# Optimization experiments

Hardware: AMD Instinct MI355X
Metric: run time of the kernel (lower is better)

Reference implementation:

```python
import jax, jax.numpy as jnp
import numpy as np

V, E, T_MAX, H, L = 20000, 384, 512, 8, 8
D = E // H  # head size 48
FF = 4 * E


def setup_inputs() -> dict:
    key = jax.random.key(0)
    ks = jax.random.split(key, 24)
    B, T = 16, 512
    s = 0.02
    return {
        "index": jax.random.randint(ks[0], (B, T), 0, V, dtype=jnp.int64),
        "targets": jax.random.randint(ks[1], (B, T), 0, V, dtype=jnp.int64),
        "tok_emb": s * jax.random.normal(ks[2], (V, E), jnp.float32),
        "pos_emb": s * jax.random.normal(ks[3], (T_MAX, E), jnp.float32),
        "Wq": s * jax.random.normal(ks[4], (L, E, H, D), jnp.float32),
        "bq": jnp.zeros((L, H, D), jnp.float32),
        "Wk": s * jax.random.normal(ks[5], (L, E, H, D), jnp.float32),
        "bk": jnp.zeros((L, H, D), jnp.float32),
        "Wv": s * jax.random.normal(ks[6], (L, E, H, D), jnp.float32),
        "bv": jnp.zeros((L, H, D), jnp.float32),
        "Wo": s * jax.random.normal(ks[7], (L, E, E), jnp.float32),
        "bo": jnp.zeros((L, E), jnp.float32),
        "ln1_g": jnp.ones((L, E), jnp.float32),
        "ln1_b": jnp.zeros((L, E), jnp.float32),
        "ln2_g": jnp.ones((L, E), jnp.float32),
        "ln2_b": jnp.zeros((L, E), jnp.float32),
        "W1": s * jax.random.normal(ks[8], (L, E, FF), jnp.float32),
        "b1": jnp.zeros((L, FF), jnp.float32),
        "W2": s * jax.random.normal(ks[9], (L, FF, E), jnp.float32),
        "b2": jnp.zeros((L, E), jnp.float32),
        "lnf_g": jnp.ones((E,), jnp.float32),
        "lnf_b": jnp.zeros((E,), jnp.float32),
        "lm_b": jnp.zeros((V,), jnp.float32),
    }


def layernorm(x, g, b, eps=1e-5):
    mu = jnp.mean(x, axis=-1, keepdims=True)
    var = jnp.var(x, axis=-1, keepdims=True)
    return (x - mu) * jax.lax.rsqrt(var + eps) * g + b


def reference(index, targets, tok_emb, pos_emb, Wq, bq, Wk, bk, Wv, bv, Wo, bo,
              ln1_g, ln1_b, ln2_g, ln2_b, W1, b1, W2, b2, lnf_g, lnf_b, lm_b):
    B, T = index.shape
    x = tok_emb[index] + pos_emb[:T]  # [B,T,E]
    causal = jnp.tril(jnp.ones((T, T), bool))
    scale = D ** -0.5
    for l in range(L):
        h = layernorm(x, ln1_g[l], ln1_b[l])
        q = jnp.einsum('bte,ehd->bthd', h, Wq[l]) + bq[l]
        k = jnp.einsum('bte,ehd->bthd', h, Wk[l]) + bk[l]
        v = jnp.einsum('bte,ehd->bthd', h, Wv[l]) + bv[l]
        scores = jnp.einsum('bqhd,bkhd->bhqk', q, k) * scale
        scores = jnp.where(causal, scores, -jnp.inf)
        w = jax.nn.softmax(scores, axis=-1)
        attn = jnp.einsum('bhqk,bkhd->bqhd', w, v).reshape(B, T, E)
        x = x + attn @ Wo[l] + bo[l]
        h2 = layernorm(x, ln2_g[l], ln2_b[l])
        ff = jax.nn.gelu(h2 @ W1[l] + b1[l], approximate=False) @ W2[l] + b2[l]
        x = x + ff
    x = layernorm(x, lnf_g, lnf_b)
    logits = x @ tok_emb.T + lm_b  # tied weights
    logits = logits.reshape(B * T, V)
    logp = jax.nn.log_softmax(logits, axis=-1)
    loss = -jnp.mean(jnp.take_along_axis(logp, targets.reshape(-1, 1), axis=-1))
    return logits, loss
```

## Files before the change

### kernel.cpp

```cpp
#include <hip/hip_runtime.h>
#include <hip/hip_bf16.h>
#include <math.h>

#define M_ROWS 8192
#define E_DIM 384
#define FF_DIM 1536
#define V_DIM 20000
#define VPAD 20096
#define N_LAYER 8
#define QK_SCALE 0.14433756729740643f
#define PSTRIDE 320

typedef __bf16 bf16x8 __attribute__((ext_vector_type(8)));
typedef short  s16x8  __attribute__((ext_vector_type(8)));
typedef float  f32x4  __attribute__((ext_vector_type(4)));
typedef __hip_bfloat16 bf16_t;

__device__ __forceinline__ void gl2lds16(const void* g, void* l) {
    __builtin_amdgcn_global_load_lds((const __attribute__((address_space(1))) void*)g,
                                     (__attribute__((address_space(3))) void*)l, 16, 0, 0);
}
__device__ __forceinline__ unsigned short bf16bits(float v) {
    return __builtin_bit_cast(unsigned short, __float2bfloat16(v));
}

__global__ __launch_bounds__(256) void tconv_kernel(
    const float* __restrict__ in, bf16_t* __restrict__ out,
    int K, int N, int outRows, int rowoff)
{
    __shared__ float tile[32][33];
    const int n0 = blockIdx.x * 32, k0 = blockIdx.y * 32;
    const float* ip = in + (size_t)blockIdx.z * K * N;
    bf16_t* op = out + (size_t)blockIdx.z * outRows * K;
    const int tx = threadIdx.x & 31, ty = threadIdx.x >> 5;
#pragma unroll
    for (int i = 0; i < 32; i += 8)
        tile[ty + i][tx] = ip[(size_t)(k0 + ty + i) * N + n0 + tx];
    __syncthreads();
#pragma unroll
    for (int i = 0; i < 32; i += 8)
        op[(size_t)(rowoff + n0 + ty + i) * K + k0 + tx] = __float2bfloat16(tile[tx][ty + i]);
}

__global__ __launch_bounds__(256) void tokconv_kernel(
    const float* __restrict__ tok, bf16_t* __restrict__ out)
{
    const size_t total = (size_t)VPAD * E_DIM;
    for (size_t i = blockIdx.x * 256ull + threadIdx.x; i < total; i += gridDim.x * 256ull) {
        int row = (int)(i / E_DIM);
        int col = (int)(i - (size_t)row * E_DIM);
        float v = (row < V_DIM) ? tok[(size_t)row * E_DIM + col] : 0.f;
        out[i] = __float2bfloat16(v);
    }
}

__global__ __launch_bounds__(256) void bqkv_kernel(
    const float* __restrict__ bq, const float* __restrict__ bk,
    const float* __restrict__ bv, float* __restrict__ o)
{
    int i = blockIdx.x * 256 + threadIdx.x;
    if (i < N_LAYER * 1152) {
        int l = i / 1152, c = i - l * 1152;
        float v = (c < 384) ? bq[l * 384 + c] : (c < 768) ? bk[l * 384 + c - 384] : bv[l * 384 + c - 768];
        o[i] = v;
    }
}

__global__ __launch_bounds__(256) void embed_kernel(
    const int* __restrict__ idx, const float* __restrict__ tok,
    const float* __restrict__ pos, float* __restrict__ x)
{
    int row = blockIdx.x * 4 + (threadIdx.x >> 6);
    int lane = threadIdx.x & 63;
    int t = row & 511;
    int id = idx[row];
    const float* tr = tok + (size_t)id * E_DIM;
    const float* pr = pos + (size_t)t * E_DIM;
    float* xr = x + (size_t)row * E_DIM;
#pragma unroll
    for (int i = 0; i < 6; i++) { int c = lane + i * 64; xr[c] = tr[c] + pr[c]; }
}

__global__ __launch_bounds__(256) void ln_kernel(
    const float* __restrict__ x, const float* __restrict__ g,
    const float* __restrict__ b, bf16_t* __restrict__ out)
{
    int row = blockIdx.x * 4 + (threadIdx.x >> 6);
    int lane = threadIdx.x & 63;
    const float* xr = x + (size_t)row * E_DIM;
    float vals[6];
    float s = 0.f;
#pragma unroll
    for (int i = 0; i < 6; i++) { vals[i] = xr[lane + i * 64]; s += vals[i]; }
#pragma unroll
    for (int off = 1; off < 64; off <<= 1) s += __shfl_xor(s, off);
    float mu = s * (1.f / E_DIM);
    float sq = 0.f;
#pragma unroll
    for (int i = 0; i < 6; i++) { float d = vals[i] - mu; sq += d * d; }
#pragma unroll
    for (int off = 1; off < 64; off <<= 1) sq += __shfl_xor(sq, off);
    float rstd = rsqrtf(sq * (1.f / E_DIM) + 1e-5f);
    bf16_t* orow = out + (size_t)row * E_DIM;
#pragma unroll
    for (int i = 0; i < 6; i++) {
        int c = lane + i * 64;
        orow[c] = __float2bfloat16((vals[i] - mu) * rstd * g[c] + b[c]);
    }
}

template <int MODE, int MREP, bool SWAP>
__global__ __launch_bounds__(256) void gemm_kernel(
    const bf16_t* __restrict__ A, const bf16_t* __restrict__ Bt,
    const float* __restrict__ bias, void* __restrict__ Cv, void* __restrict__ C2,
    int Ncols, int K)
{
    constexpr int BMR = MREP * 32;
    __shared__ __align__(16) short smem[8192];
    const int t = threadIdx.x;
    const int w = t >> 6, lane = t & 63;
    const int wm = w >> 1, wn = w & 1;
    const int bm = (MODE == 3 ? blockIdx.x : blockIdx.y) * BMR;
    const int bn = (MODE == 3 ? blockIdx.y : blockIdx.x) * 128;

    f32x4 acc[MREP][4];
#pragma unroll
    for (int m = 0; m < MREP; m++)
#pragma unroll
        for (int n = 0; n < 4; n++)
            acc[m][n] = (f32x4){0.f, 0.f, 0.f, 0.f};

    const int lg = lane >> 4;
    const int ll = lane & 15;

    for (int kt = 0; kt < K; kt += 32) {
        __syncthreads();
#pragma unroll
        for (int i = 0; i < MREP / 2; i++) {
            int li = i * 256 + t;
            int g = li >> (MREP == 4 ? 7 : 6);
            int row = li & (BMR - 1);
            gl2lds16(A + (size_t)(bm + row) * K + kt + g * 8,
                     smem + (size_t)(i * 256 + w * 64) * 8);
        }
#pragma unroll
        for (int i = 0; i < 2; i++) {
            int li = i * 256 + t;
            gl2lds16(Bt + (size_t)(bn + (li & 127)) * K + kt + (li >> 7) * 8,
                     smem + 4096 + (size_t)(i * 256 + w * 64) * 8);
        }
        asm volatile("s_waitcnt vmcnt(0)" ::: "memory");
        __syncthreads();

        bf16x8 af[MREP], bfr[4];
#pragma unroll
        for (int m = 0; m < MREP; m++)
            af[m] = __builtin_bit_cast(bf16x8,
                *(const s16x8*)&smem[(lg * BMR + wm * (BMR / 2) + m * 16 + ll) * 8]);
#pragma unroll
        for (int n = 0; n < 4; n++)
            bfr[n] = __builtin_bit_cast(bf16x8,
                *(const s16x8*)&smem[4096 + (lg * 128 + wn * 64 + n * 16 + ll) * 8]);
#pragma unroll
        for (int m = 0; m < MREP; m++)
#pragma unroll
            for (int n = 0; n < 4; n++) {
                if (SWAP)
                    acc[m][n] = __builtin_amdgcn_mfma_f32_16x16x32_bf16(bfr[n], af[m], acc[m][n], 0, 0, 0);
                else
                    acc[m][n] = __builtin_amdgcn_mfma_f32_16x16x32_bf16(af[m], bfr[n], acc[m][n], 0, 0, 0);
            }
    }

    if constexpr (SWAP) {
        const int rowm0 = bm + wm * (BMR / 2) + ll;
        const int coln0 = bn + wn * 64 + lg * 4;

        if constexpr (MODE == 4) {
            bf16_t* qkvb = (bf16_t*)Cv;
            const float sc = (bn >= 384) ? 1.f : QK_SCALE;
#pragma unroll
            for (int n = 0; n < 4; n++) {
                const int coln = coln0 + n * 16;
                const float4 b4 = *(const float4*)&bias[coln];
#pragma unroll
                for (int m = 0; m < MREP; m++) {
                    const int row = rowm0 + m * 16;
                    ushort4 pk;
                    pk.x = bf16bits((acc[m][n][0] + b4.x) * sc);
                    pk.y = bf16bits((acc[m][n][1] + b4.y) * sc);
                    pk.z = bf16bits((acc[m][n][2] + b4.z) * sc);
                    pk.w = bf16bits((acc[m][n][3] + b4.w) * sc);
                    *(ushort4*)&qkvb[(size_t)row * 1152 + coln] = pk;
                }
            }
        } else if constexpr (MODE == 1) {
            float* C = (float*)Cv;
#pragma unroll
            for (int n = 0; n < 4; n++) {
                const int coln = coln0 + n * 16;
                const float4 b4 = *(const float4*)&bias[coln];
#pragma unroll
                for (int m = 0; m < MREP; m++) {
                    const int row = rowm0 + m * 16;
                    float4 cv = *(float4*)&C[(size_t)row * Ncols + coln];
                    cv.x += acc[m][n][0] + b4.x;
                    cv.y += acc[m][n][1] + b4.y;
                    cv.z += acc[m][n][2] + b4.z;
                    cv.w += acc[m][n][3] + b4.w;
                    *(float4*)&C[(size_t)row * Ncols + coln] = cv;
                }
            }
        } else if constexpr (MODE == 2) {
            bf16_t* O = (bf16_t*)Cv;
#pragma unroll
            for (int n = 0; n < 4; n++) {
                const int coln = coln0 + n * 16;
                const float4 b4 = *(const float4*)&bias[coln];
#pragma unroll
                for (int m = 0; m < MREP; m++) {
                    const int row = rowm0 + m * 16;
                    float v0 = acc[m][n][0] + b4.x, v1 = acc[m][n][1] + b4.y;
                    float v2 = acc[m][n][2] + b4.z, v3 = acc[m][n][3] + b4.w;
                    v0 = 0.5f * v0 * (1.f + erff(v0 * 0.70710678118654752f));
                    v1 = 0.5f * v1 * (1.f + erff(v1 * 0.70710678118654752f));
                    v2 = 0.5f * v2 * (1.f + erff(v2 * 0.70710678118654752f));
                    v3 = 0.5f * v3 * (1.f + erff(v3 * 0.70710678118654752f));
                    ushort4 pk;
                    pk.x = bf16bits(v0); pk.y = bf16bits(v1);
                    pk.z = bf16bits(v2); pk.w = bf16bits(v3);
                    *(ushort4*)&O[(size_t)row * Ncols + coln] = pk;
                }
            }
        } else if constexpr (MODE == 3) {
            float* C = (float*)Cv;
            float* pbuf = (float*)C2;
            const int ptile = blockIdx.y * 2 + wn;
#pragma unroll
            for (int m = 0; m < MREP; m++) {
                const int row = rowm0 + m * 16;
                float se = 0.f;
#pragma unroll
                for (int n = 0; n < 4; n++) {
                    const int coln = coln0 + n * 16;
                    if (coln + 3 < Ncols) {
                        const float4 b4 = *(const float4*)&bias[coln];
                        float4 v;
                        v.x = acc[m][n][0] + b4.x;
                        v.y = acc[m][n][1] + b4.y;
                        v.z = acc[m][n][2] + b4.z;
                        v.w = acc[m][n][3] + b4.w;
                        *(float4*)&C[(size_t)row * Ncols + coln] = v;
                        se += __expf(v.x) + __expf(v.y) + __expf(v.z) + __expf(v.w);
                    } else {
#pragma unroll
                        for (int e = 0; e < 4; e++) {
                            int col = coln + e;
                            if (col < Ncols) {
                                float v = acc[m][n][e] + bias[col];
                                C[(size_t)row * Ncols + col] = v;
                                se += __expf(v);
                            }
                        }
                    }
                }
                se += __shfl_xor(se, 16);
                se += __shfl_xor(se, 32);
                if (lg == 0) pbuf[(size_t)row * PSTRIDE + ptile] = se;
            }
        }
        return;
    }

    {
        const int r0 = bm + wm * (BMR / 2) + lg * 4;
        const int c0 = bn + wn * 64 + ll;
        bf16_t* vtb = (bf16_t*)C2;
#pragma unroll
        for (int n = 0; n < 4; n++) {
            const int col = c0 + n * 16;
            const float bv = bias[col];
            const int hh = col / 48, dd = col - hh * 48;
#pragma unroll
            for (int m = 0; m < MREP; m++) {
                const int row0 = r0 + m * 16;
                const int bb = row0 >> 9, tt2 = row0 & 511;
                ushort4 pk;
                pk.x = bf16bits(acc[m][n][0] + bv);
                pk.y = bf16bits(acc[m][n][1] + bv);
                pk.z = bf16bits(acc[m][n][2] + bv);
                pk.w = bf16bits(acc[m][n][3] + bv);
                *(ushort4*)&vtb[((size_t)(bb * 8 + hh) * 48 + dd) * 512 + tt2] = pk;
            }
        }
    }
}

__global__ __launch_bounds__(256) void attn_kernel(
    const bf16_t* __restrict__ qkvb, const bf16_t* __restrict__ vt,
    bf16_t* __restrict__ o)
{
    const int qt = blockIdx.x, bh = blockIdx.y;
    const int b = bh >> 3, h = bh & 7;
    __shared__ unsigned short psm[4608];
    const int tid = threadIdx.x;
    const int w = tid >> 6, lane = tid & 63;
    const int ll = lane & 15, g = lane >> 4;
    const int q0 = qt * 64;
    const int q_abs = q0 + ll * 4 + w;

    const bf16_t* qrow = qkvb + (size_t)(b * 512 + q_abs) * 1152 + h * 48;
    bf16x8 qf0 = __builtin_bit_cast(bf16x8, *(const s16x8*)(qrow + g * 8));
    bf16x8 qf1 = {};
    if (g < 2) qf1 = __builtin_bit_cast(bf16x8, *(const s16x8*)(qrow + 32 + g * 8));

    f32x4 oacc[3];
#pragma unroll
    for (int df = 0; df < 3; df++) oacc[df] = (f32x4){0.f, 0.f, 0.f, 0.f};
    float mrun = -1e30f, ssum = 0.f;

    const bf16_t* kb0 = qkvb + (size_t)b * 512 * 1152 + 384 + h * 48;
    const bf16_t* vb0 = vt + (size_t)bh * 48 * 512;
    const int ntiles = 2 * (qt + 1);

    for (int kt = 0; kt < ntiles; kt++) {
        const int kbase = kt * 32;
        f32x4 sfr[2];
#pragma unroll
        for (int f = 0; f < 2; f++) {
            const bf16_t* krow = kb0 + (size_t)(kbase + f * 16 + ll) * 1152;
            bf16x8 k0 = __builtin_bit_cast(bf16x8, *(const s16x8*)(krow + g * 8));
            bf16x8 k1 = {};
            if (g < 2) k1 = __builtin_bit_cast(bf16x8, *(const s16x8*)(krow + 32 + g * 8));
            f32x4 z = {0.f, 0.f, 0.f, 0.f};
            z = __builtin_amdgcn_mfma_f32_16x16x32_bf16(k0, qf0, z, 0, 0, 0);
            z = __builtin_amdgcn_mfma_f32_16x16x32_bf16(k1, qf1, z, 0, 0, 0);
            sfr[f] = z;
        }
        bf16x8 vf[3];
#pragma unroll
        for (int df = 0; df < 3; df++)
            vf[df] = __builtin_bit_cast(bf16x8,
                *(const s16x8*)(vb0 + (size_t)(df * 16 + ll) * 512 + kbase + g * 8));

        float p[8];
        float tmax = -1e30f;
#pragma unroll
        for (int f = 0; f < 2; f++)
#pragma unroll
            for (int j = 0; j < 4; j++) {
                int key = kbase + f * 16 + g * 4 + j;
                float sv = sfr[f][j];
                sv = (key > q_abs) ? -1e30f : sv;
                p[f * 4 + j] = sv;
                tmax = fmaxf(tmax, sv);
            }
        tmax = fmaxf(tmax, __shfl_xor(tmax, 16));
        tmax = fmaxf(tmax, __shfl_xor(tmax, 32));
        float mnew = fmaxf(mrun, tmax);
        float corr = __expf(mrun - mnew);
        float psum = 0.f;
#pragma unroll
        for (int i = 0; i < 8; i++) { p[i] = __expf(p[i] - mnew); psum += p[i]; }
        psum += __shfl_xor(psum, 16);
        psum += __shfl_xor(psum, 32);
        ssum = ssum * corr + psum;
        mrun = mnew;
#pragma unroll
        for (int df = 0; df < 3; df++)
#pragma unroll
            for (int j = 0; j < 4; j++) oacc[df][j] *= corr;

        const int pbase = (w * 2 + (kt & 1)) * 576;
#pragma unroll
        for (int f = 0; f < 2; f++)
#pragma unroll
            for (int j = 0; j < 4; j++)
                psm[pbase + (f * 16 + g * 4 + j) * 18 + ll] =
                    __builtin_bit_cast(unsigned short, __float2bfloat16(p[f * 4 + j]));
        s16x8 pr;
#pragma unroll
        for (int i = 0; i < 8; i++)
            pr[i] = (short)psm[pbase + (g * 8 + i) * 18 + ll];
        bf16x8 pf = __builtin_bit_cast(bf16x8, pr);
#pragma unroll
        for (int df = 0; df < 3; df++)
            oacc[df] = __builtin_amdgcn_mfma_f32_16x16x32_bf16(vf[df], pf, oacc[df], 0, 0, 0);
    }

    float inv = 1.f / ssum;
    bf16_t* orow = o + (size_t)(b * 512 + q_abs) * 384 + h * 48;
#pragma unroll
    for (int df = 0; df < 3; df++) {
        ushort4 pk;
        pk.x = bf16bits(oacc[df][0] * inv);
        pk.y = bf16bits(oacc[df][1] * inv);
        pk.z = bf16bits(oacc[df][2] * inv);
        pk.w = bf16bits(oacc[df][3] * inv);
        *(ushort4*)&orow[df * 16 + g * 4] = pk;
    }
}

__global__ __launch_bounds__(256) void loss_row2_kernel(
    const float* __restrict__ pbuf, const float* __restrict__ logits,
    const int* __restrict__ targets, float* __restrict__ rowloss)
{
    int row = blockIdx.x * 4 + (threadIdx.x >> 6);
    int lane = threadIdx.x & 63;
    const float* pr = pbuf + (size_t)row * PSTRIDE;
    float s = 0.f;
    for (int i = lane; i < 314; i += 64) s += pr[i];
#pragma unroll
    for (int off = 1; off < 64; off <<= 1) s += __shfl_xor(s, off);
    if (lane == 0) {
        int tgt = targets[row];
        rowloss[row] = logf(s) - logits[(size_t)row * V_DIM + tgt];
    }
}

__global__ __launch_bounds__(256) void loss_reduce_kernel(
    const float* __restrict__ rowloss, float* __restrict__ out)
{
    int t = threadIdx.x;
    __shared__ float red[4];
    float s = 0.f;
    for (int i = t; i < M_ROWS; i += 256) s += rowloss[i];
#pragma unroll
    for (int off = 1; off < 64; off <<= 1) s += __shfl_xor(s, off);
    if ((t & 63) == 0) red[t >> 6] = s;
    __syncthreads();
    if (t == 0) out[0] = (red[0] + red[1] + red[2] + red[3]) * (1.f / M_ROWS);
}

extern "C" void kernel_launch(void* const* d_in, const int* in_sizes, int n_in,
                              void* d_out, int out_size, void* d_ws, size_t ws_size,
                              hipStream_t stream)
{
    const int*   index   = (const int*)d_in[0];
    const int*   targets = (const int*)d_in[1];
    const float* tok_emb = (const float*)d_in[2];
    const float* pos_emb = (const float*)d_in[3];
    const float* Wq = (const float*)d_in[4];
    const float* bq = (const float*)d_in[5];
    const float* Wk = (const float*)d_in[6];
    const float* bk = (const float*)d_in[7];
    const float* Wv = (const float*)d_in[8];
    const float* bv = (const float*)d_in[9];
    const float* Wo = (const float*)d_in[10];
    const float* bo = (const float*)d_in[11];
    const float* ln1_g = (const float*)d_in[12];
    const float* ln1_b = (const float*)d_in[13];
    const float* ln2_g = (const float*)d_in[14];
    const float* ln2_b = (const float*)d_in[15];
    const float* W1 = (const float*)d_in[16];
    const float* b1 = (const float*)d_in[17];
    const float* W2 = (const float*)d_in[18];
    const float* b2 = (const float*)d_in[19];
    const float* lnf_g = (const float*)d_in[20];
    const float* lnf_b = (const float*)d_in[21];
    const float* lm_b  = (const float*)d_in[22];

    float* out = (float*)d_out;
    char* wsb = (char*)d_ws;

    float*  x     = (float*)(wsb + 0);
    bf16_t* hbuf  = (bf16_t*)(wsb + 12582912);
    bf16_t* obuf  = (bf16_t*)(wsb + 18874368);
    bf16_t* qkvb  = (bf16_t*)(wsb + 25165824);
    bf16_t* vtb   = (bf16_t*)(wsb + 44040192);
    bf16_t* ffmid = (bf16_t*)(wsb + 18874368);
    bf16_t* tokb  = (bf16_t*)(wsb + 50331648);
    bf16_t* qkvw  = (bf16_t*)(wsb + 65765376);
    bf16_t* wo_t  = (bf16_t*)(wsb + 72843264);
    bf16_t* w1_t  = (bf16_t*)(wsb + 75202560);
    bf16_t* w2_t  = (bf16_t*)(wsb + 84639744);
    float*  bqkv  = (float*)(wsb + 94076928);
    float*  rowloss = (float*)(wsb + 94113792);
    float*  pbuf  = (float*)(wsb + 94146560);

    tokconv_kernel<<<2048, 256, 0, stream>>>(tok_emb, tokb);
    tconv_kernel<<<dim3(12, 12, 8), 256, 0, stream>>>(Wq, qkvw, 384, 384, 1152, 0);
    tconv_kernel<<<dim3(12, 12, 8), 256, 0, stream>>>(Wk, qkvw, 384, 384, 1152, 384);
    tconv_kernel<<<dim3(12, 12, 8), 256, 0, stream>>>(Wv, qkvw, 384, 384, 1152, 768);
    tconv_kernel<<<dim3(12, 12, 8), 256, 0, stream>>>(Wo, wo_t, 384, 384, 384, 0);
    tconv_kernel<<<dim3(48, 12, 8), 256, 0, stream>>>(W1, w1_t, 384, 1536, 1536, 0);
    tconv_kernel<<<dim3(12, 48, 8), 256, 0, stream>>>(W2, w2_t, 1536, 384, 384, 0);
    bqkv_kernel<<<36, 256, 0, stream>>>(bq, bk, bv, bqkv);

    embed_kernel<<<2048, 256, 0, stream>>>(index, tok_emb, pos_emb, x);

    for (int l = 0; l < N_LAYER; l++) {
        const bf16_t* qkvw_l = qkvw + (size_t)l * 1152 * 384;
        const float*  bqkv_l = bqkv + l * 1152;
        ln_kernel<<<2048, 256, 0, stream>>>(x, ln1_g + l * E_DIM, ln1_b + l * E_DIM, hbuf);
        gemm_kernel<4, 4, true><<<dim3(6, 64), 256, 0, stream>>>(
            hbuf, qkvw_l, bqkv_l, qkvb, nullptr, 1152, 384);
        gemm_kernel<5, 4, false><<<dim3(3, 64), 256, 0, stream>>>(
            hbuf, qkvw_l + (size_t)768 * 384, bqkv_l + 768, nullptr, vtb, 384, 384);
        attn_kernel<<<dim3(8, 128), 256, 0, stream>>>(qkvb, vtb, obuf);
        gemm_kernel<1, 2, true><<<dim3(3, 128), 256, 0, stream>>>(
            obuf, wo_t + (size_t)l * 384 * 384, bo + l * E_DIM, x, nullptr, 384, 384);
        ln_kernel<<<2048, 256, 0, stream>>>(x, ln2_g + l * E_DIM, ln2_b + l * E_DIM, hbuf);
        gemm_kernel<2, 4, true><<<dim3(12, 64), 256, 0, stream>>>(
            hbuf, w1_t + (size_t)l * 1536 * 384, b1 + l * FF_DIM, ffmid, nullptr, 1536, 384);
        gemm_kernel<1, 2, true><<<dim3(3, 128), 256, 0, stream>>>(
            ffmid, w2_t + (size_t)l * 384 * 1536, b2 + l * E_DIM, x, nullptr, 384, 1536);
    }

    ln_kernel<<<2048, 256, 0, stream>>>(x, lnf_g, lnf_b, hbuf);
    gemm_kernel<3, 4, true><<<dim3(64, 157), 256, 0, stream>>>(
        hbuf, tokb, lm_b, out, pbuf, V_DIM, 384);

    loss_row2_kernel<<<2048, 256, 0, stream>>>(pbuf, out, targets, rowloss);
    loss_reduce_kernel<<<1, 256, 0, stream>>>(rowloss, out + (size_t)M_ROWS * V_DIM);
}
```

Measured before the change: 1.995 ms.

## Add dedicated logits kernel keeping A tile resident in LDS across vocab tiles

Replaces the generic GEMM for the final vocab projection with a kernel that loads the full 64x384 row block of normalized activations into LDS once, then loops over up to four 128-column vocab tiles, streaming only the tied-embedding tiles. The fused bias, logit store and per-tile exp-sum partials are kept, now written per wave, which doubles the partial count, so the row-loss kernel sums more entries. The partial-sum buffer moves into a reused workspace region. The aim is to cut repeated A reloads and raise reuse. The cost is 64KB of LDS per block, which limits occupancy, and no overlap of loads with compute.

```diff
diff --git a/kernel.cpp b/kernel.cpp
--- a/kernel.cpp
+++ b/kernel.cpp
@@ -9,7 +9,8 @@
 #define VPAD 20096
 #define N_LAYER 8
 #define QK_SCALE 0.14433756729740643f
-#define PSTRIDE 320
+#define PSTRIDE 640
+#define NPART 628
 
 typedef __bf16 bf16x8 __attribute__((ext_vector_type(8)));
 typedef short  s16x8  __attribute__((ext_vector_type(8)));
@@ -120,8 +121,8 @@
     const int t = threadIdx.x;
     const int w = t >> 6, lane = t & 63;
     const int wm = w >> 1, wn = w & 1;
-    const int bm = (MODE == 3 ? blockIdx.x : blockIdx.y) * BMR;
-    const int bn = (MODE == 3 ? blockIdx.y : blockIdx.x) * 128;
+    const int bm = blockIdx.y * BMR;
+    const int bn = blockIdx.x * 128;
 
     f32x4 acc[MREP][4];
 #pragma unroll
@@ -232,42 +233,6 @@
                     *(ushort4*)&O[(size_t)row * Ncols + coln] = pk;
                 }
             }
-        } else if constexpr (MODE == 3) {
-            float* C = (float*)Cv;
-            float* pbuf = (float*)C2;
-            const int ptile = blockIdx.y * 2 + wn;
-#pragma unroll
-            for (int m = 0; m < MREP; m++) {
-                const int row = rowm0 + m * 16;
-                float se = 0.f;
-#pragma unroll
-                for (int n = 0; n < 4; n++) {
-                    const int coln = coln0 + n * 16;
-                    if (coln + 3 < Ncols) {
-                        const float4 b4 = *(const float4*)&bias[coln];
-                        float4 v;
-                        v.x = acc[m][n][0] + b4.x;
-                        v.y = acc[m][n][1] + b4.y;
-                        v.z = acc[m][n][2] + b4.z;
-                        v.w = acc[m][n][3] + b4.w;
-                        *(float4*)&C[(size_t)row * Ncols + coln] = v;
-                        se += __expf(v.x) + __expf(v.y) + __expf(v.z) + __expf(v.w);
-                    } else {
-#pragma unroll
-                        for (int e = 0; e < 4; e++) {
-                            int col = coln + e;
-                            if (col < Ncols) {
-                                float v = acc[m][n][e] + bias[col];
-                                C[(size_t)row * Ncols + col] = v;
-                                se += __expf(v);
-                            }
-                        }
-                    }
-                }
-                se += __shfl_xor(se, 16);
-                se += __shfl_xor(se, 32);
-                if (lg == 0) pbuf[(size_t)row * PSTRIDE + ptile] = se;
-            }
         }
         return;
     }
@@ -296,6 +261,108 @@
     }
 }
 
+__global__ __launch_bounds__(256) void logits_kernel(
+    const bf16_t* __restrict__ A, const bf16_t* __restrict__ Bt,
+    const float* __restrict__ bias, float* __restrict__ C,
+    float* __restrict__ pbuf)
+{
+    __shared__ __align__(16) short smem[32768];
+    const int t = threadIdx.x;
+    const int w = t >> 6, lane = t & 63;
+    const int lg = lane >> 4, ll = lane & 15;
+    const int bm = blockIdx.x * 64;
+    const int bnsup = blockIdx.y;
+    const int bn0 = bnsup * 512;
+    const int ntiles = (bnsup < 39) ? 4 : 1;
+
+#pragma unroll
+    for (int i = 0; i < 12; i++) {
+        int c = i * 256 + t;
+        int kg = c >> 6, row = c & 63;
+        gl2lds16(A + (size_t)(bm + row) * E_DIM + kg * 8,
+                 smem + (size_t)(i * 256 + w * 64) * 8);
+    }
+    asm volatile("s_waitcnt vmcnt(0)" ::: "memory");
+    __syncthreads();
+
+    short* smB = smem + 24576;
+    for (int bnl = 0; bnl < ntiles; bnl++) {
+        const int tb = bn0 + bnl * 128;
+        f32x4 acc[4][2];
+#pragma unroll
+        for (int m = 0; m < 4; m++)
+#pragma unroll
+            for (int nf = 0; nf < 2; nf++)
+                acc[m][nf] = (f32x4){0.f, 0.f, 0.f, 0.f};
+
+        for (int kt = 0; kt < 6; kt++) {
+            __syncthreads();
+#pragma unroll
+            for (int i = 0; i < 4; i++) {
+                int c = i * 256 + t;
+                int kg = c >> 7, col = c & 127;
+                gl2lds16(Bt + (size_t)(tb + col) * E_DIM + kt * 64 + kg * 8,
+                         smB + (size_t)(i * 256 + w * 64) * 8);
+            }
+            asm volatile("s_waitcnt vmcnt(0)" ::: "memory");
+            __syncthreads();
+#pragma unroll
+            for (int kk = 0; kk < 2; kk++) {
+                bf16x8 af[4], bfr[2];
+#pragma unroll
+                for (int m = 0; m < 4; m++)
+                    af[m] = __builtin_bit_cast(bf16x8,
+                        *(const s16x8*)&smem[((kt * 8 + kk * 4 + lg) * 64 + m * 16 + ll) * 8]);
+#pragma unroll
+                for (int nf = 0; nf < 2; nf++)
+                    bfr[nf] = __builtin_bit_cast(bf16x8,
+                        *(const s16x8*)&smB[((kk * 4 + lg) * 128 + w * 32 + nf * 16 + ll) * 8]);
+#pragma unroll
+                for (int m = 0; m < 4; m++)
+#pragma unroll
+                    for (int nf = 0; nf < 2; nf++)
+                        acc[m][nf] = __builtin_amdgcn_mfma_f32_16x16x32_bf16(
+                            bfr[nf], af[m], acc[m][nf], 0, 0, 0);
+            }
+        }
+
+        const int cn0 = tb + w * 32 + lg * 4;
+        const int pidx = bnsup * 16 + bnl * 4 + w;
+#pragma unroll
+        for (int m = 0; m < 4; m++) {
+            const int row = bm + m * 16 + ll;
+            float se = 0.f;
+#pragma unroll
+            for (int nf = 0; nf < 2; nf++) {
+                const int cn = cn0 + nf * 16;
+                if (cn + 3 < V_DIM) {
+                    const float4 b4 = *(const float4*)&bias[cn];
+                    float4 v;
+                    v.x = acc[m][nf][0] + b4.x;
+                    v.y = acc[m][nf][1] + b4.y;
+                    v.z = acc[m][nf][2] + b4.z;
+                    v.w = acc[m][nf][3] + b4.w;
+                    *(float4*)&C[(size_t)row * V_DIM + cn] = v;
+                    se += __expf(v.x) + __expf(v.y) + __expf(v.z) + __expf(v.w);
+                } else {
+#pragma unroll
+                    for (int e = 0; e < 4; e++) {
+                        int col = cn + e;
+                        if (col < V_DIM) {
+                            float v = acc[m][nf][e] + bias[col];
+                            C[(size_t)row * V_DIM + col] = v;
+                            se += __expf(v);
+                        }
+                    }
+                }
+            }
+            se += __shfl_xor(se, 16);
+            se += __shfl_xor(se, 32);
+            if (lg == 0) pbuf[(size_t)row * PSTRIDE + pidx] = se;
+        }
+    }
+}
+
 __global__ __launch_bounds__(256) void attn_kernel(
     const bf16_t* __restrict__ qkvb, const bf16_t* __restrict__ vt,
     bf16_t* __restrict__ o)
@@ -409,7 +476,7 @@
     int lane = threadIdx.x & 63;
     const float* pr = pbuf + (size_t)row * PSTRIDE;
     float s = 0.f;
-    for (int i = lane; i < 314; i += 64) s += pr[i];
+    for (int i = lane; i < NPART; i += 64) s += pr[i];
 #pragma unroll
     for (int off = 1; off < 64; off <<= 1) s += __shfl_xor(s, off);
     if (lane == 0) {
@@ -469,6 +536,7 @@
     bf16_t* qkvb  = (bf16_t*)(wsb + 25165824);
     bf16_t* vtb   = (bf16_t*)(wsb + 44040192);
     bf16_t* ffmid = (bf16_t*)(wsb + 18874368);
+    float*  pbuf  = (float*)(wsb + 25165824);
     bf16_t* tokb  = (bf16_t*)(wsb + 50331648);
     bf16_t* qkvw  = (bf16_t*)(wsb + 65765376);
     bf16_t* wo_t  = (bf16_t*)(wsb + 72843264);
@@ -476,7 +544,6 @@
     bf16_t* w2_t  = (bf16_t*)(wsb + 84639744);
     float*  bqkv  = (float*)(wsb + 94076928);
     float*  rowloss = (float*)(wsb + 94113792);
-    float*  pbuf  = (float*)(wsb + 94146560);
 
     tokconv_kernel<<<2048, 256, 0, stream>>>(tok_emb, tokb);
     tconv_kernel<<<dim3(12, 12, 8), 256, 0, stream>>>(Wq, qkvw, 384, 384, 1152, 0);
@@ -508,8 +575,7 @@
     }
 
     ln_kernel<<<2048, 256, 0, stream>>>(x, lnf_g, lnf_b, hbuf);
-    gemm_kernel<3, 4, true><<<dim3(64, 157), 256, 0, stream>>>(
-        hbuf, tokb, lm_b, out, pbuf, V_DIM, 384);
+    logits_kernel<<<dim3(128, 40), 256, 0, stream>>>(hbuf, tokb, lm_b, out, pbuf);
 
     loss_row2_kernel<<<2048, 256, 0, stream>>>(pbuf, out, targets, rowloss);
     loss_reduce_kernel<<<1, 256, 0, stream>>>(rowloss, out + (size_t)M_ROWS * V_DIM);
```

Measured after the change: 2.148 ms. +7.7%, slower.
